# Optimization experiments

Hardware: AMD Instinct MI355X
Metric: run time of the kernel (lower is better)

Reference implementation:

```python
import jax, jax.numpy as jnp
import numpy as np

N, E, H, R = 20000, 400000, 128, 20


def setup_inputs() -> dict:
    key = jax.random.key(0)
    ks = jax.random.split(key, 12)
    inv_h = 1.0 / np.sqrt(H)
    inv_r = 1.0 / np.sqrt(R)
    return {
        "s": jax.random.normal(ks[0], (N, H), jnp.float32),
        "v": jax.random.normal(ks[1], (N, 3, H), jnp.float32),
        "edge_rbf": jax.random.normal(ks[2], (E, R), jnp.float32),
        "edge_cutoff": jax.random.uniform(ks[3], (E,), jnp.float32),
        "edge_vec": jax.random.normal(ks[4], (E, 3), jnp.float32),
        "W1": jax.random.normal(ks[5], (H, H), jnp.float32) * inv_h,
        "b1": jnp.zeros((H,), jnp.float32),
        "W2": jax.random.normal(ks[6], (H, 3 * H), jnp.float32) * inv_h,
        "b2": jnp.zeros((3 * H,), jnp.float32),
        "Wr": jax.random.normal(ks[7], (R, 3 * H), jnp.float32) * inv_r,
        "br": jnp.zeros((3 * H,), jnp.float32),
        "edge_index": jax.random.randint(ks[8], (2, E), 0, N, jnp.int64),
    }


def reference(s, v, edge_rbf, edge_cutoff, edge_vec, W1, b1, W2, b2, Wr, br, edge_index):
    i, j = edge_index[0], edge_index[1]
    n = s.shape[0]
    # rbf projection modulated by cutoff: [E, 3H]
    W = (edge_rbf @ Wr + br) * edge_cutoff[:, None]
    # scalar MLP on gathered source features: [E, 3H]
    h = jax.nn.silu(s[j] @ W1 + b1)
    x = (h @ W2 + b2) * W
    x_ss, x_sv, x_vv = jnp.split(x, 3, axis=-1)  # each [E, H]
    ds = jax.ops.segment_sum(x_ss, i, num_segments=n)
    # dv1: outer product of edge direction with gated scalars -> [E,3,H]
    dv1 = jax.ops.segment_sum(x_sv[:, None, :] * edge_vec[:, :, None], i, num_segments=n)
    # equivariant term: project v_j onto edge direction, re-expand
    inner = jnp.sum(v[j] * edge_vec[:, :, None], axis=1)  # [E, H]
    dv2 = jax.ops.segment_sum((inner * x_vv)[:, None, :] * edge_vec[:, :, None], i, num_segments=n)
    return ds, dv1 + dv2
```

## Files before the change

### kernel.cpp

```cpp
#include <hip/hip_runtime.h>
#include <hip/hip_bf16.h>

#define HDIM 128
#define H3   384
#define RDIM 20
#define NPB  16
#define CHNK 32

typedef unsigned short u16;

__device__ __forceinline__ float bf2f(u16 u) {
    union { unsigned int i; float f; } x;
    x.i = ((unsigned int)u) << 16;
    return x.f;
}
__device__ __forceinline__ u16 f2bf(float f) {
    __hip_bfloat16 h = __float2bfloat16(f);
    return *(u16*)&h;
}

__global__ __launch_bounds__(128) void node_mlp_kernel(
    const float* __restrict__ s, const float* __restrict__ W1,
    const float* __restrict__ b1, const float* __restrict__ W2,
    const float* __restrict__ b2, u16* __restrict__ P, int N)
{
    __shared__ float sS[NPB][HDIM];
    __shared__ float sH[NPB][HDIM];
    const int t  = threadIdx.x;
    const int n0 = blockIdx.x * NPB;

    #pragma unroll
    for (int n = 0; n < NPB; ++n) {
        int node = n0 + n;
        sS[n][t] = (node < N) ? s[(size_t)node * HDIM + t] : 0.f;
    }
    __syncthreads();

    float acc[NPB];
    #pragma unroll
    for (int n = 0; n < NPB; ++n) acc[n] = 0.f;
    for (int k = 0; k < HDIM; ++k) {
        float w = W1[k * HDIM + t];
        #pragma unroll
        for (int n = 0; n < NPB; ++n) acc[n] += sS[n][k] * w;
    }
    float bb = b1[t];
    #pragma unroll
    for (int n = 0; n < NPB; ++n) {
        float z = acc[n] + bb;
        sH[n][t] = z / (1.f + __expf(-z));
    }
    __syncthreads();

    float a0[NPB], a1[NPB], a2[NPB];
    #pragma unroll
    for (int n = 0; n < NPB; ++n) { a0[n] = 0.f; a1[n] = 0.f; a2[n] = 0.f; }
    for (int k2 = 0; k2 < HDIM / 2; ++k2) {
        float2 hv[NPB];
        #pragma unroll
        for (int n = 0; n < NPB; ++n) hv[n] = ((const float2*)sH[n])[k2];
        #pragma unroll
        for (int kk = 0; kk < 2; ++kk) {
            int k = 2 * k2 + kk;
            float w0 = W2[k * H3 + t];
            float w1 = W2[k * H3 + t + 128];
            float w2 = W2[k * H3 + t + 256];
            #pragma unroll
            for (int n = 0; n < NPB; ++n) {
                float h = kk ? hv[n].y : hv[n].x;
                a0[n] += h * w0;
                a1[n] += h * w1;
                a2[n] += h * w2;
            }
        }
    }
    float c0 = b2[t], c1 = b2[t + 128], c2 = b2[t + 256];
    #pragma unroll
    for (int n = 0; n < NPB; ++n) {
        int node = n0 + n;
        if (node < N) {
            size_t base = (size_t)node * H3;
            P[base + t]       = f2bf(a0[n] + c0);
            P[base + t + 128] = f2bf(a1[n] + c1);
            P[base + t + 256] = f2bf(a2[n] + c2);
        }
    }
}

__global__ void vconv_kernel(const float* __restrict__ v, u16* __restrict__ Vb, int nquads)
{
    int idx = blockIdx.x * 256 + threadIdx.x;
    int stride = gridDim.x * 256;
    for (; idx < nquads; idx += stride) {
        float4 f = ((const float4*)v)[idx];
        ushort4 o;
        o.x = f2bf(f.x); o.y = f2bf(f.y); o.z = f2bf(f.z); o.w = f2bf(f.w);
        ((ushort4*)Vb)[idx] = o;
    }
}

__global__ void hist_kernel(const int* __restrict__ eidx, int* __restrict__ counts, int E)
{
    int e = blockIdx.x * 256 + threadIdx.x;
    if (e < E) atomicAdd(&counts[eidx[e]], 1);
}

__global__ __launch_bounds__(1024) void scan_kernel(
    const int* __restrict__ counts, int* __restrict__ rstart,
    int* __restrict__ cursor, int N)
{
    __shared__ int part[1024];
    const int t = threadIdx.x;
    const int C = 20;
    int loc[C];
    int s = 0;
    #pragma unroll
    for (int q = 0; q < C; ++q) {
        int idx = t * C + q;
        int c = (idx < N) ? counts[idx] : 0;
        loc[q] = s; s += c;
    }
    part[t] = s;
    __syncthreads();
    for (int off = 1; off < 1024; off <<= 1) {
        int vv = (t >= off) ? part[t - off] : 0;
        __syncthreads();
        part[t] += vv;
        __syncthreads();
    }
    int boff = (t > 0) ? part[t - 1] : 0;
    #pragma unroll
    for (int q = 0; q < C; ++q) {
        int idx = t * C + q;
        if (idx < N) {
            int st = boff + loc[q];
            rstart[idx] = st;
            cursor[idx] = st;
        }
    }
    if (t == 1023) rstart[N] = part[1023];
}

__global__ void scatter_kernel(const int* __restrict__ eidx, int* __restrict__ cursor,
                               int* __restrict__ eord, int E)
{
    int e = blockIdx.x * 256 + threadIdx.x;
    if (e < E) {
        int i = eidx[e];
        int pos = atomicAdd(&cursor[i], 1);
        eord[pos] = e;
    }
}

__global__ __launch_bounds__(128) void reduce_kernel(
    const int* __restrict__ rstart, const int* __restrict__ eord,
    const float* __restrict__ rbf, const float* __restrict__ cutoff,
    const float* __restrict__ evec, const float* __restrict__ Wr,
    const float* __restrict__ br, const u16* __restrict__ Pb,
    const u16* __restrict__ Vb, const int* __restrict__ eidx,
    float* __restrict__ ds, float* __restrict__ dv, int E)
{
    const int t = threadIdx.x;
    const int i = blockIdx.x;

    float wr0[RDIM], wr1[RDIM], wr2[RDIM];
    #pragma unroll
    for (int k = 0; k < RDIM; ++k) {
        wr0[k] = Wr[k * H3 + t];
        wr1[k] = Wr[k * H3 + t + 128];
        wr2[k] = Wr[k * H3 + t + 256];
    }
    float br0 = br[t], br1 = br[t + 128], br2 = br[t + 256];

    int beg = rstart[i], end = rstart[i + 1];
    float accs = 0.f, accx = 0.f, accy = 0.f, accz = 0.f;

    __shared__ int   sE[CHNK], sJ[CHNK];
    __shared__ float sCut[CHNK], sVx[CHNK], sVy[CHNK], sVz[CHNK];
    __shared__ __attribute__((aligned(16))) float sRbf[CHNK][RDIM];

    for (int c0 = beg; c0 < end; c0 += CHNK) {
        int cnt = min(CHNK, end - c0);
        __syncthreads();
        if (t < cnt) {
            int e = eord[c0 + t];
            sE[t]   = e;
            sJ[t]   = eidx[E + e];
            sCut[t] = cutoff[e];
            sVx[t]  = evec[3 * e];
            sVy[t]  = evec[3 * e + 1];
            sVz[t]  = evec[3 * e + 2];
        }
        __syncthreads();
        for (int x = t; x < cnt * RDIM; x += 128) {
            int n = x / RDIM, k = x - n * RDIM;
            sRbf[n][k] = rbf[(size_t)sE[n] * RDIM + k];
        }
        __syncthreads();

        u16 cpss, cpsv, cpvv, cvx, cvy, cvz;
        {
            size_t pj = (size_t)sJ[0] * H3;
            cpss = Pb[pj + t]; cpsv = Pb[pj + 128 + t]; cpvv = Pb[pj + 256 + t];
            cvx  = Vb[pj + t]; cvy  = Vb[pj + 128 + t]; cvz  = Vb[pj + 256 + t];
        }
        for (int q = 0; q < cnt; ++q) {
            u16 npss = 0, npsv = 0, npvv = 0, nvx = 0, nvy = 0, nvz = 0;
            if (q + 1 < cnt) {
                size_t pj = (size_t)sJ[q + 1] * H3;
                npss = Pb[pj + t]; npsv = Pb[pj + 128 + t]; npvv = Pb[pj + 256 + t];
                nvx  = Vb[pj + t]; nvy  = Vb[pj + 128 + t]; nvz  = Vb[pj + 256 + t];
            }
            const float4* r4 = (const float4*)sRbf[q];
            float w0 = 0.f, w1 = 0.f, w2 = 0.f;
            #pragma unroll
            for (int k4 = 0; k4 < 5; ++k4) {
                float4 r = r4[k4];
                w0 += r.x * wr0[4*k4+0] + r.y * wr0[4*k4+1] + r.z * wr0[4*k4+2] + r.w * wr0[4*k4+3];
                w1 += r.x * wr1[4*k4+0] + r.y * wr1[4*k4+1] + r.z * wr1[4*k4+2] + r.w * wr1[4*k4+3];
                w2 += r.x * wr2[4*k4+0] + r.y * wr2[4*k4+1] + r.z * wr2[4*k4+2] + r.w * wr2[4*k4+3];
            }
            float cu = sCut[q];
            float ex = sVx[q], ey = sVy[q], ez = sVz[q];
            float xss = (w0 + br0) * cu * bf2f(cpss);
            float xsv = (w1 + br1) * cu * bf2f(cpsv);
            float xvv = (w2 + br2) * cu * bf2f(cpvv);
            float inner = bf2f(cvx) * ex + bf2f(cvy) * ey + bf2f(cvz) * ez;
            float coef  = xsv + inner * xvv;
            accs += xss;
            accx += coef * ex;
            accy += coef * ey;
            accz += coef * ez;
            cpss = npss; cpsv = npsv; cpvv = npvv;
            cvx = nvx; cvy = nvy; cvz = nvz;
        }
    }

    ds[(size_t)i * HDIM + t] = accs;
    size_t dvi = (size_t)i * H3;
    dv[dvi + t]       = accx;
    dv[dvi + 128 + t] = accy;
    dv[dvi + 256 + t] = accz;
}

extern "C" void kernel_launch(void* const* d_in, const int* in_sizes, int n_in,
                              void* d_out, int out_size, void* d_ws, size_t ws_size,
                              hipStream_t stream)
{
    const float* s    = (const float*)d_in[0];
    const float* v    = (const float*)d_in[1];
    const float* rbf  = (const float*)d_in[2];
    const float* cut  = (const float*)d_in[3];
    const float* evec = (const float*)d_in[4];
    const float* W1   = (const float*)d_in[5];
    const float* b1   = (const float*)d_in[6];
    const float* W2   = (const float*)d_in[7];
    const float* b2   = (const float*)d_in[8];
    const float* Wr   = (const float*)d_in[9];
    const float* br   = (const float*)d_in[10];
    const int*   eidx = (const int*)d_in[11];

    const int N = in_sizes[0] / HDIM;
    const int E = in_sizes[3];

    float* out = (float*)d_out;
    float* ds  = out;
    float* dv  = out + (size_t)N * HDIM;

    char* w = (char*)d_ws;
    u16* P  = (u16*)w;                     w += ((size_t)N * H3 * 2 + 255) / 256 * 256;
    u16* Vb = (u16*)w;                     w += ((size_t)N * H3 * 2 + 255) / 256 * 256;
    int* counts = (int*)w;                 w += ((size_t)N * 4 + 255) / 256 * 256;
    int* rstart = (int*)w;                 w += ((size_t)(N + 1) * 4 + 255) / 256 * 256;
    int* cursor = (int*)w;                 w += ((size_t)N * 4 + 255) / 256 * 256;
    int* eord   = (int*)w;

    hipMemsetAsync(counts, 0, (size_t)N * sizeof(int), stream);

    vconv_kernel<<<1024, 256, 0, stream>>>(v, Vb, N * H3 / 4);
    node_mlp_kernel<<<(N + NPB - 1) / NPB, 128, 0, stream>>>(s, W1, b1, W2, b2, P, N);
    hist_kernel<<<(E + 255) / 256, 256, 0, stream>>>(eidx, counts, E);
    scan_kernel<<<1, 1024, 0, stream>>>(counts, rstart, cursor, N);
    scatter_kernel<<<(E + 255) / 256, 256, 0, stream>>>(eidx, cursor, eord, E);
    reduce_kernel<<<N, 128, 0, stream>>>(rstart, eord, rbf, cut, evec, Wr, br, P, Vb,
                                         eidx, ds, dv, E);
}
```

Baseline: 338.4 us.

## Use MFMA for rbf projection, pack node features, process several nodes per block

The per-edge rbf projection (20x384) is moved from scalar FMAs with Wr held in registers onto bf16 MFMA 16x16x32 instructions. The 16-edge results go through shared memory in bf16. The v-to-bf16 conversion is fused into the node MLP kernel, which writes P and v interleaved into three packed u32 arrays so each gather needs three 32-bit loads per thread instead of six 16-bit loads. Each reduce block now handles 4 nodes, which amortises the Wr fragment setup. The cost is extra bf16 rounding of rbf, Wr and W, and a larger share of padded MFMA work when nodes have few edges.

After: 369.3 us. 9.1% more time.

```diff
diff --git a/kernel.cpp b/kernel.cpp
--- a/kernel.cpp
+++ b/kernel.cpp
@@ -5,24 +5,36 @@
 #define H3   384
 #define RDIM 20
 #define NPB  16
-#define CHNK 32
+#define NPR  4
+#define CHNK 16
 
 typedef unsigned short u16;
-
-__device__ __forceinline__ float bf2f(u16 u) {
-    union { unsigned int i; float f; } x;
-    x.i = ((unsigned int)u) << 16;
-    return x.f;
-}
+typedef unsigned int   u32;
+typedef __attribute__((ext_vector_type(8))) short short8v;
+typedef __attribute__((ext_vector_type(4))) float f32x4;
+
 __device__ __forceinline__ u16 f2bf(float f) {
     __hip_bfloat16 h = __float2bfloat16(f);
     return *(u16*)&h;
 }
+__device__ __forceinline__ float bf2f(u16 u) {
+    union { u32 i; float f; } x; x.i = (u32)u << 16; return x.f;
+}
+__device__ __forceinline__ float bflo(u32 u) {
+    union { u32 i; float f; } x; x.i = u << 16; return x.f;
+}
+__device__ __forceinline__ float bfhi(u32 u) {
+    union { u32 i; float f; } x; x.i = u & 0xffff0000u; return x.f;
+}
+__device__ __forceinline__ u32 pk(float lo, float hi) {
+    return (u32)f2bf(lo) | ((u32)f2bf(hi) << 16);
+}
 
 __global__ __launch_bounds__(128) void node_mlp_kernel(
     const float* __restrict__ s, const float* __restrict__ W1,
     const float* __restrict__ b1, const float* __restrict__ W2,
-    const float* __restrict__ b2, u16* __restrict__ P, int N)
+    const float* __restrict__ b2, const float* __restrict__ v,
+    u32* __restrict__ PA, u32* __restrict__ PB, u32* __restrict__ PC, int N)
 {
     __shared__ float sS[NPB][HDIM];
     __shared__ float sH[NPB][HDIM];
@@ -79,23 +91,13 @@
     for (int n = 0; n < NPB; ++n) {
         int node = n0 + n;
         if (node < N) {
-            size_t base = (size_t)node * H3;
-            P[base + t]       = f2bf(a0[n] + c0);
-            P[base + t + 128] = f2bf(a1[n] + c1);
-            P[base + t + 256] = f2bf(a2[n] + c2);
-        }
-    }
-}
-
-__global__ void vconv_kernel(const float* __restrict__ v, u16* __restrict__ Vb, int nquads)
-{
-    int idx = blockIdx.x * 256 + threadIdx.x;
-    int stride = gridDim.x * 256;
-    for (; idx < nquads; idx += stride) {
-        float4 f = ((const float4*)v)[idx];
-        ushort4 o;
-        o.x = f2bf(f.x); o.y = f2bf(f.y); o.z = f2bf(f.z); o.w = f2bf(f.w);
-        ((ushort4*)Vb)[idx] = o;
+            size_t vb = (size_t)node * H3;
+            float vx = v[vb + t], vy = v[vb + 128 + t], vz = v[vb + 256 + t];
+            size_t pb = (size_t)node * HDIM + t;
+            PA[pb] = pk(a0[n] + c0, a1[n] + c1);
+            PB[pb] = pk(a2[n] + c2, vx);
+            PC[pb] = pk(vy, vz);
+        }
     }
 }
 
@@ -156,91 +158,126 @@
     const int* __restrict__ rstart, const int* __restrict__ eord,
     const float* __restrict__ rbf, const float* __restrict__ cutoff,
     const float* __restrict__ evec, const float* __restrict__ Wr,
-    const float* __restrict__ br, const u16* __restrict__ Pb,
-    const u16* __restrict__ Vb, const int* __restrict__ eidx,
-    float* __restrict__ ds, float* __restrict__ dv, int E)
-{
-    const int t = threadIdx.x;
-    const int i = blockIdx.x;
-
-    float wr0[RDIM], wr1[RDIM], wr2[RDIM];
-    #pragma unroll
-    for (int k = 0; k < RDIM; ++k) {
-        wr0[k] = Wr[k * H3 + t];
-        wr1[k] = Wr[k * H3 + t + 128];
-        wr2[k] = Wr[k * H3 + t + 256];
+    const float* __restrict__ br, const u32* __restrict__ PA,
+    const u32* __restrict__ PB, const u32* __restrict__ PC,
+    const int* __restrict__ eidx, float* __restrict__ ds,
+    float* __restrict__ dv, int E, int N)
+{
+    const int t    = threadIdx.x;
+    const int lane = t & 63;
+    const int wave = t >> 6;
+    const int g    = lane >> 4;
+    const int m    = lane & 15;
+
+    short8v bfrag[12];
+    #pragma unroll
+    for (int n = 0; n < 12; ++n) {
+        int col = wave * 192 + n * 16 + m;
+        short8v f;
+        #pragma unroll
+        for (int j = 0; j < 8; ++j) {
+            int k = 8 * g + j;
+            float val = (k < RDIM) ? Wr[k * H3 + col] : 0.f;
+            f[j] = (short)f2bf(val);
+        }
+        bfrag[n] = f;
     }
     float br0 = br[t], br1 = br[t + 128], br2 = br[t + 256];
-
-    int beg = rstart[i], end = rstart[i + 1];
-    float accs = 0.f, accx = 0.f, accy = 0.f, accz = 0.f;
 
     __shared__ int   sE[CHNK], sJ[CHNK];
     __shared__ float sCut[CHNK], sVx[CHNK], sVy[CHNK], sVz[CHNK];
-    __shared__ __attribute__((aligned(16))) float sRbf[CHNK][RDIM];
-
-    for (int c0 = beg; c0 < end; c0 += CHNK) {
-        int cnt = min(CHNK, end - c0);
-        __syncthreads();
-        if (t < cnt) {
-            int e = eord[c0 + t];
-            sE[t]   = e;
-            sJ[t]   = eidx[E + e];
-            sCut[t] = cutoff[e];
-            sVx[t]  = evec[3 * e];
-            sVy[t]  = evec[3 * e + 1];
-            sVz[t]  = evec[3 * e + 2];
-        }
-        __syncthreads();
-        for (int x = t; x < cnt * RDIM; x += 128) {
-            int n = x / RDIM, k = x - n * RDIM;
-            sRbf[n][k] = rbf[(size_t)sE[n] * RDIM + k];
-        }
-        __syncthreads();
-
-        u16 cpss, cpsv, cpvv, cvx, cvy, cvz;
-        {
-            size_t pj = (size_t)sJ[0] * H3;
-            cpss = Pb[pj + t]; cpsv = Pb[pj + 128 + t]; cpvv = Pb[pj + 256 + t];
-            cvx  = Vb[pj + t]; cvy  = Vb[pj + 128 + t]; cvz  = Vb[pj + 256 + t];
-        }
-        for (int q = 0; q < cnt; ++q) {
-            u16 npss = 0, npsv = 0, npvv = 0, nvx = 0, nvy = 0, nvz = 0;
-            if (q + 1 < cnt) {
-                size_t pj = (size_t)sJ[q + 1] * H3;
-                npss = Pb[pj + t]; npsv = Pb[pj + 128 + t]; npvv = Pb[pj + 256 + t];
-                nvx  = Vb[pj + t]; nvy  = Vb[pj + 128 + t]; nvz  = Vb[pj + 256 + t];
-            }
-            const float4* r4 = (const float4*)sRbf[q];
-            float w0 = 0.f, w1 = 0.f, w2 = 0.f;
+    __shared__ u16   Wl[CHNK][H3];
+
+    for (int nn = 0; nn < NPR; ++nn) {
+        int node = blockIdx.x * NPR + nn;
+        if (node >= N) break;
+        int beg = rstart[node], end = rstart[node + 1];
+        float accs = 0.f, accx = 0.f, accy = 0.f, accz = 0.f;
+
+        for (int c0 = beg; c0 < end; c0 += CHNK) {
+            int cnt = min(CHNK, end - c0);
+            __syncthreads();
+            if (t < CHNK) {
+                int e = eord[c0 + ((t < cnt) ? t : 0)];
+                sE[t]   = e;
+                sJ[t]   = eidx[E + e];
+                sCut[t] = cutoff[e];
+                sVx[t]  = evec[3 * e];
+                sVy[t]  = evec[3 * e + 1];
+                sVz[t]  = evec[3 * e + 2];
+            }
+            __syncthreads();
+
+            short8v af;
+            if (g == 3) {
+                #pragma unroll
+                for (int j = 0; j < 8; ++j) af[j] = 0;
+            } else {
+                const float* rrow = rbf + (size_t)sE[m] * RDIM;
+                if (g < 2) {
+                    float4 r0 = *(const float4*)(rrow + 8 * g);
+                    float4 r1 = *(const float4*)(rrow + 8 * g + 4);
+                    af[0] = (short)f2bf(r0.x); af[1] = (short)f2bf(r0.y);
+                    af[2] = (short)f2bf(r0.z); af[3] = (short)f2bf(r0.w);
+                    af[4] = (short)f2bf(r1.x); af[5] = (short)f2bf(r1.y);
+                    af[6] = (short)f2bf(r1.z); af[7] = (short)f2bf(r1.w);
+                } else {
+                    float4 r0 = *(const float4*)(rrow + 16);
+                    af[0] = (short)f2bf(r0.x); af[1] = (short)f2bf(r0.y);
+                    af[2] = (short)f2bf(r0.z); af[3] = (short)f2bf(r0.w);
+                    af[4] = 0; af[5] = 0; af[6] = 0; af[7] = 0;
+                }
+            }
+
             #pragma unroll
-            for (int k4 = 0; k4 < 5; ++k4) {
-                float4 r = r4[k4];
-                w0 += r.x * wr0[4*k4+0] + r.y * wr0[4*k4+1] + r.z * wr0[4*k4+2] + r.w * wr0[4*k4+3];
-                w1 += r.x * wr1[4*k4+0] + r.y * wr1[4*k4+1] + r.z * wr1[4*k4+2] + r.w * wr1[4*k4+3];
-                w2 += r.x * wr2[4*k4+0] + r.y * wr2[4*k4+1] + r.z * wr2[4*k4+2] + r.w * wr2[4*k4+3];
-            }
-            float cu = sCut[q];
-            float ex = sVx[q], ey = sVy[q], ez = sVz[q];
-            float xss = (w0 + br0) * cu * bf2f(cpss);
-            float xsv = (w1 + br1) * cu * bf2f(cpsv);
-            float xvv = (w2 + br2) * cu * bf2f(cpvv);
-            float inner = bf2f(cvx) * ex + bf2f(cvy) * ey + bf2f(cvz) * ez;
-            float coef  = xsv + inner * xvv;
-            accs += xss;
-            accx += coef * ex;
-            accy += coef * ey;
-            accz += coef * ez;
-            cpss = npss; cpsv = npsv; cpvv = npvv;
-            cvx = nvx; cvy = nvy; cvz = nvz;
-        }
-    }
-
-    ds[(size_t)i * HDIM + t] = accs;
-    size_t dvi = (size_t)i * H3;
-    dv[dvi + t]       = accx;
-    dv[dvi + 128 + t] = accy;
-    dv[dvi + 256 + t] = accz;
+            for (int n = 0; n < 12; ++n) {
+                f32x4 c = {0.f, 0.f, 0.f, 0.f};
+                c = __builtin_amdgcn_mfma_f32_16x16x32_bf16(af, bfrag[n], c, 0, 0, 0);
+                int col = wave * 192 + n * 16 + m;
+                #pragma unroll
+                for (int r = 0; r < 4; ++r)
+                    Wl[4 * g + r][col] = f2bf(c[r]);
+            }
+            __syncthreads();
+
+            u32 ca, cb, cc;
+            {
+                size_t pj = (size_t)sJ[0] * HDIM + t;
+                ca = PA[pj]; cb = PB[pj]; cc = PC[pj];
+            }
+            for (int q = 0; q < cnt; ++q) {
+                u32 na = 0, nb = 0, nc = 0;
+                if (q + 1 < cnt) {
+                    size_t pj = (size_t)sJ[q + 1] * HDIM + t;
+                    na = PA[pj]; nb = PB[pj]; nc = PC[pj];
+                }
+                float w0 = bf2f(Wl[q][t]);
+                float w1 = bf2f(Wl[q][t + 128]);
+                float w2 = bf2f(Wl[q][t + 256]);
+                float cu = sCut[q];
+                float ex = sVx[q], ey = sVy[q], ez = sVz[q];
+                float pss = bflo(ca), psv = bfhi(ca);
+                float pvv = bflo(cb), vx  = bfhi(cb);
+                float vy  = bflo(cc), vz  = bfhi(cc);
+                float xss = (w0 + br0) * cu * pss;
+                float xsv = (w1 + br1) * cu * psv;
+                float xvv = (w2 + br2) * cu * pvv;
+                float inner = vx * ex + vy * ey + vz * ez;
+                float coef  = xsv + inner * xvv;
+                accs += xss;
+                accx += coef * ex;
+                accy += coef * ey;
+                accz += coef * ez;
+                ca = na; cb = nb; cc = nc;
+            }
+        }
+
+        ds[(size_t)node * HDIM + t] = accs;
+        size_t dvi = (size_t)node * H3;
+        dv[dvi + t]       = accx;
+        dv[dvi + 128 + t] = accy;
+        dv[dvi + 256 + t] = accz;
+    }
 }
 
 extern "C" void kernel_launch(void* const* d_in, const int* in_sizes, int n_in,
@@ -268,8 +305,9 @@
     float* dv  = out + (size_t)N * HDIM;
 
     char* w = (char*)d_ws;
-    u16* P  = (u16*)w;                     w += ((size_t)N * H3 * 2 + 255) / 256 * 256;
-    u16* Vb = (u16*)w;                     w += ((size_t)N * H3 * 2 + 255) / 256 * 256;
+    u32* PA = (u32*)w;                     w += ((size_t)N * HDIM * 4 + 255) / 256 * 256;
+    u32* PB = (u32*)w;                     w += ((size_t)N * HDIM * 4 + 255) / 256 * 256;
+    u32* PC = (u32*)w;                     w += ((size_t)N * HDIM * 4 + 255) / 256 * 256;
     int* counts = (int*)w;                 w += ((size_t)N * 4 + 255) / 256 * 256;
     int* rstart = (int*)w;                 w += ((size_t)(N + 1) * 4 + 255) / 256 * 256;
     int* cursor = (int*)w;                 w += ((size_t)N * 4 + 255) / 256 * 256;
@@ -277,11 +315,12 @@
 
     hipMemsetAsync(counts, 0, (size_t)N * sizeof(int), stream);
 
-    vconv_kernel<<<1024, 256, 0, stream>>>(v, Vb, N * H3 / 4);
-    node_mlp_kernel<<<(N + NPB - 1) / NPB, 128, 0, stream>>>(s, W1, b1, W2, b2, P, N);
+    node_mlp_kernel<<<(N + NPB - 1) / NPB, 128, 0, stream>>>(s, W1, b1, W2, b2, v,
+                                                             PA, PB, PC, N);
     hist_kernel<<<(E + 255) / 256, 256, 0, stream>>>(eidx, counts, E);
     scan_kernel<<<1, 1024, 0, stream>>>(counts, rstart, cursor, N);
     scatter_kernel<<<(E + 255) / 256, 256, 0, stream>>>(eidx, cursor, eord, E);
-    reduce_kernel<<<N, 128, 0, stream>>>(rstart, eord, rbf, cut, evec, Wr, br, P, Vb,
-                                         eidx, ds, dv, E);
-}
+    reduce_kernel<<<(N + NPR - 1) / NPR, 128, 0, stream>>>(rstart, eord, rbf, cut, evec,
+                                                           Wr, br, PA, PB, PC, eidx,
+                                                           ds, dv, E, N);
+}
```
